# Optimization experiments

Hardware: AMD Instinct MI355X
Metric: run time of the kernel (lower is better)

The kernel has to match this reference:

```python
import jax, jax.numpy as jnp
import numpy as np

CHUNK = 128


def setup_inputs() -> dict:
    key = jax.random.key(0)
    ks = jax.random.split(key, 10)
    B, L, d, n = 4, 2048, 192, 64
    sd = 1.0 / np.sqrt(d)
    return {
        "x": jax.random.normal(ks[0], (B, L, d), dtype=jnp.float32),
        "A_log": -jnp.log(2.0) + 0.1 * jax.random.normal(ks[1], (d,), dtype=jnp.float32),
        "W_B": sd * jax.random.normal(ks[2], (n, d), dtype=jnp.float32),
        "W_C": sd * jax.random.normal(ks[3], (n, d), dtype=jnp.float32),
        "W_dt": sd * jax.random.normal(ks[4], (d, d), dtype=jnp.float32),
        "b_dt": 0.1 * jax.random.normal(ks[5], (d,), dtype=jnp.float32),
        "W_xp": sd * jax.random.normal(ks[6], (2 * d, d), dtype=jnp.float32),
        "b_xp": 0.1 * jax.random.normal(ks[7], (2 * d,), dtype=jnp.float32),
        "W_out": sd * jax.random.normal(ks[8], (d, d), dtype=jnp.float32),
        "b_out": 0.1 * jax.random.normal(ks[9], (d,), dtype=jnp.float32),
    }


def reference(x, A_log, W_B, W_C, W_dt, b_dt, W_xp, b_xp, W_out, b_out):
    p = CHUNK
    b, l, d = x.shape
    n = W_B.shape[0]
    pad = (-l) % p
    xp = jnp.pad(x, ((0, 0), (0, pad), (0, 0))) if pad > 0 else x
    c = xp.shape[1] // p

    A = -jnp.exp(A_log)                                   # (d,)
    proj = xp @ W_xp.T + b_xp                             # (b, Lp, 2d)
    x_bar, z = jnp.split(proj, 2, axis=-1)
    Bm = x_bar @ W_B.T                                    # (b, Lp, n)
    Cm = x_bar @ W_C.T                                    # (b, Lp, n)
    dt = jax.nn.softplus(x_bar @ W_dt.T + b_dt)           # (b, Lp, d)
    A_bar = jnp.exp(dt * A)                               # (b, Lp, d)

    resh = lambda t: t.reshape(b, c, p, t.shape[-1])
    xc, Bc, Cc, Ac = resh(x_bar), resh(Bm), resh(Cm), resh(A_bar)

    # intra-chunk: masked decay matrix M[b,c,i,j,d]
    log_A = jnp.log(jnp.abs(Ac) + 1e-8)
    la_cum = jnp.cumsum(log_A, axis=2)                    # (b,c,p,d)
    log_M = la_cum[:, :, :, None, :] - la_cum[:, :, None, :, :]
    causal = jnp.tril(jnp.ones((p, p), dtype=x.dtype))
    M = jnp.exp(log_M) * causal[None, None, :, :, None]   # (b,c,p,p,d)
    G = jnp.einsum('bcin,bcjn->bcij', Cc, Bc)             # C_i . B_j
    # same math as einsum('bcpn,bcpnd->bcpd', C, einsum('bcijd,bcjnd->bcind', M, B x))
    y_intra = jnp.einsum('bcij,bcijd,bcjd->bcid', G, M, xc)

    # inter-chunk recurrence over chunk states
    chunk_A = jnp.prod(Ac, axis=2)                        # (b,c,d)
    chunk_states = jnp.einsum('bcpn,bcpd->bcnd', Bc, xc * Ac)

    def step(state, inp):
        ca, cs = inp                                       # (b,d), (b,n,d)
        return state * ca[:, None, :] + cs, state          # emit state BEFORE update

    _, prev = jax.lax.scan(
        step,
        jnp.zeros((b, n, d), dtype=x.dtype),
        (jnp.moveaxis(chunk_A, 1, 0), jnp.moveaxis(chunk_states, 1, 0)),
    )
    prev = jnp.moveaxis(prev, 0, 1)                       # (b,c,n,d)
    y_inter = jnp.einsum('bcpn,bcnd->bcpd', Cc, prev)

    y = (y_intra + y_inter).reshape(b, c * p, d)[:, :l]
    y = y * jax.nn.silu(z[:, :l])
    return y @ W_out.T + b_out
```

## Files before the change

kernel.cpp:

```cpp
#include <hip/hip_runtime.h>
#include <math.h>

#define TOK      8192
#define DIM      192
#define NST      64
#define PCHUNK   128
#define NCHUNKS  64
#define CPB      16
#define BATCH    4
#define SUB      32
#define NSUB     4
#define NG2      2
#define NPG2     32

typedef __attribute__((ext_vector_type(8))) short  bf16x8;
typedef __attribute__((ext_vector_type(4))) float  f32x4;

__device__ __forceinline__ unsigned short f2bf(float f) {
    unsigned int u = __float_as_uint(f);
    u += 0x7fff + ((u >> 16) & 1);
    return (unsigned short)(u >> 16);
}

__global__ __launch_bounds__(256)
void cast_kernel(const float* __restrict__ x,   const float* __restrict__ Wxp,
                 const float* __restrict__ WB,  const float* __restrict__ WC,
                 const float* __restrict__ Wdt, const float* __restrict__ Wout,
                 unsigned short* __restrict__ xb,     unsigned short* __restrict__ wxpb,
                 unsigned short* __restrict__ wbcdtb, unsigned short* __restrict__ woutb)
{
    int u = blockIdx.x * 256 + threadIdx.x;
    const float* src; unsigned short* dst; int idx;
    if      (u < 393216) { src = x;    dst = xb;             idx = u; }
    else if (u < 411648) { src = Wxp;  dst = wxpb;           idx = u - 393216; }
    else if (u < 414720) { src = WB;   dst = wbcdtb;         idx = u - 411648; }
    else if (u < 417792) { src = WC;   dst = wbcdtb + 12288; idx = u - 414720; }
    else if (u < 427008) { src = Wdt;  dst = wbcdtb + 24576; idx = u - 417792; }
    else if (u < 436224) { src = Wout; dst = woutb;          idx = u - 427008; }
    else return;
    float4 v = *(const float4*)(src + (size_t)idx * 4);
    ushort4 r; r.x = f2bf(v.x); r.y = f2bf(v.y); r.z = f2bf(v.z); r.w = f2bf(v.w);
    *(ushort4*)(dst + (size_t)idx * 4) = r;
}

__device__ __forceinline__
void mfma_64x64(const unsigned short* __restrict__ X, int ldx,
                const unsigned short* __restrict__ W, int K,
                int m_wave, int n0, int lr, int kg, f32x4 acc[4][4])
{
    for (int k0 = 0; k0 < K; k0 += 32) {
        bf16x8 af[4], bfr[4];
        #pragma unroll
        for (int mi = 0; mi < 4; ++mi)
            af[mi] = *(const bf16x8*)(X + (size_t)(m_wave + mi*16 + lr) * ldx + k0 + kg*8);
        #pragma unroll
        for (int ni = 0; ni < 4; ++ni)
            bfr[ni] = *(const bf16x8*)(W + (size_t)(n0 + ni*16 + lr) * K + k0 + kg*8);
        #pragma unroll
        for (int mi = 0; mi < 4; ++mi)
            #pragma unroll
            for (int ni = 0; ni < 4; ++ni)
                acc[mi][ni] = __builtin_amdgcn_mfma_f32_16x16x32_bf16(
                                  af[mi], bfr[ni], acc[mi][ni], 0, 0, 0);
    }
}

__global__ __launch_bounds__(256)
void proj_gemm(const unsigned short* __restrict__ xb,
               const unsigned short* __restrict__ wxpb,
               const float* __restrict__ b_xp,
               float* __restrict__ proj, unsigned short* __restrict__ projb)
{
    const int lane = threadIdx.x & 63, wave = threadIdx.x >> 6;
    const int m_wave = blockIdx.x * 256 + wave * 64;
    const int n0 = blockIdx.y * 64;
    const int lr = lane & 15, kg = lane >> 4;
    f32x4 acc[4][4] = {};
    mfma_64x64(xb, DIM, wxpb, DIM, m_wave, n0, lr, kg, acc);
    #pragma unroll
    for (int ni = 0; ni < 4; ++ni) {
        int col = n0 + ni*16 + lr;
        float bias = b_xp[col];
        #pragma unroll
        for (int mi = 0; mi < 4; ++mi)
            #pragma unroll
            for (int r = 0; r < 4; ++r) {
                int row = m_wave + mi*16 + kg*4 + r;
                float v = acc[mi][ni][r] + bias;
                proj [(size_t)row * 384 + col] = v;
                projb[(size_t)row * 384 + col] = f2bf(v);
            }
    }
}

__global__ __launch_bounds__(256)
void bcdt_gemm(const unsigned short* __restrict__ projb,
               const unsigned short* __restrict__ wbcdtb,
               const float* __restrict__ b_dt, const float* __restrict__ A_log,
               float* __restrict__ BC, float* __restrict__ Abar)
{
    const int lane = threadIdx.x & 63, wave = threadIdx.x >> 6;
    const int m_wave = blockIdx.x * 256 + wave * 64;
    const int n0 = blockIdx.y * 64;
    const int lr = lane & 15, kg = lane >> 4;
    f32x4 acc[4][4] = {};
    mfma_64x64(projb, 384, wbcdtb, DIM, m_wave, n0, lr, kg, acc);
    if (n0 < 128) {
        #pragma unroll
        for (int ni = 0; ni < 4; ++ni) {
            int col = n0 + ni*16 + lr;
            #pragma unroll
            for (int mi = 0; mi < 4; ++mi)
                #pragma unroll
                for (int r = 0; r < 4; ++r) {
                    int row = m_wave + mi*16 + kg*4 + r;
                    BC[(size_t)row * 128 + col] = acc[mi][ni][r];
                }
        }
    } else {
        #pragma unroll
        for (int ni = 0; ni < 4; ++ni) {
            int c2 = n0 - 128 + ni*16 + lr;
            float bias = b_dt[c2];
            float Av = -expf(A_log[c2]);
            #pragma unroll
            for (int mi = 0; mi < 4; ++mi)
                #pragma unroll
                for (int r = 0; r < 4; ++r) {
                    int row = m_wave + mi*16 + kg*4 + r;
                    float v = acc[mi][ni][r] + bias;
                    float sp = (v > 20.f) ? v : log1pf(expf(v));
                    Abar[(size_t)row * DIM + c2] = expf(sp * Av);
                }
        }
    }
}

__global__ __launch_bounds__(256)
void out_gemm(const unsigned short* __restrict__ ygb,
              const unsigned short* __restrict__ woutb,
              const float* __restrict__ b_out, float* __restrict__ out)
{
    const int lane = threadIdx.x & 63, wave = threadIdx.x >> 6;
    const int m_wave = blockIdx.x * 256 + wave * 64;
    const int n0 = blockIdx.y * 64;
    const int lr = lane & 15, kg = lane >> 4;
    f32x4 acc[4][4] = {};
    mfma_64x64(ygb, DIM, woutb, DIM, m_wave, n0, lr, kg, acc);
    #pragma unroll
    for (int ni = 0; ni < 4; ++ni) {
        int col = n0 + ni*16 + lr;
        float bias = b_out[col];
        #pragma unroll
        for (int mi = 0; mi < 4; ++mi)
            #pragma unroll
            for (int r = 0; r < 4; ++r) {
                int row = m_wave + mi*16 + kg*4 + r;
                out[(size_t)row * DIM + col] = acc[mi][ni][r] + bias;
            }
    }
}

__global__ __launch_bounds__(192)
void state_kernel(const float* __restrict__ proj,
                  const float* __restrict__ Abar,
                  const float* __restrict__ Bm,
                  float* __restrict__ S,
                  float* __restrict__ R,
                  float* __restrict__ dprod)
{
    int bc = blockIdx.x, s = blockIdx.y, g = blockIdx.z;
    int dd = threadIdx.x;
    int t0 = bc * PCHUNK + s * SUB;
    __shared__ float Bs[SUB][NPG2];
    for (int idx = threadIdx.x; idx < SUB * NPG2; idx += 192) {
        int i = idx >> 5, j = idx & 31;
        Bs[i][j] = Bm[(size_t)(t0 + i) * 128 + g * NPG2 + j];
    }
    __syncthreads();
    float H[NPG2] = {}, Rr[NPG2] = {};
    float cp = 1.f;
    float a_cur = fabsf(Abar[(size_t)t0 * DIM + dd]) + 1e-8f;
    float x_cur = proj[(size_t)t0 * 384 + dd];
    for (int i = 0; i < SUB; ++i) {
        float a_nxt = 0.f, x_nxt = 0.f;
        if (i + 1 < SUB) {
            a_nxt = fabsf(Abar[(size_t)(t0 + i + 1) * DIM + dd]) + 1e-8f;
            x_nxt = proj[(size_t)(t0 + i + 1) * 384 + dd];
        }
        cp *= a_cur;
        #pragma unroll
        for (int j = 0; j < NPG2; ++j) {
            float u = Bs[i][j] * x_cur;
            H[j]  = fmaf(a_cur, H[j], u);
            Rr[j] = fmaf(u, a_cur, Rr[j]);
        }
        a_cur = a_nxt; x_cur = x_nxt;
    }
    size_t base = (((size_t)(bc * NSUB + s)) * NST + g * NPG2) * DIM + dd;
    #pragma unroll
    for (int j = 0; j < NPG2; ++j) {
        S[base + (size_t)j * DIM] = H[j];
        R[base + (size_t)j * DIM] = Rr[j];
    }
    if (g == 0) dprod[(size_t)(bc * NSUB + s) * DIM + dd] = cp;
}

__global__ __launch_bounds__(256)
void scan_kernel(const float* __restrict__ dprod,
                 const float* __restrict__ R,
                 float* __restrict__ prev)
{
    int v = blockIdx.x * 256 + threadIdx.x;
    if (v >= BATCH * NST * 48) return;
    int dd = (v % 48) * 4;
    int nn = (v / 48) % NST;
    int b  = v / (48 * NST);
    const size_t Q2 = (size_t)NST * DIM;
    float4 st = {0.f, 0.f, 0.f, 0.f};
    for (int c = 0; c < CPB; ++c) {
        int bc = b * CPB + c;
        size_t so = ((size_t)(bc * NSUB) * NST + nn) * DIM + dd;
        float4 Rs = {0.f, 0.f, 0.f, 0.f};
        float4 cA = {1.f, 1.f, 1.f, 1.f};
        #pragma unroll
        for (int s = 0; s < NSUB; ++s) {
            float4 dp = *(const float4*)(dprod + (size_t)(bc * NSUB + s) * DIM + dd);
            float4 Rv = *(const float4*)(R + so + (size_t)s * Q2);
            cA.x *= dp.x; cA.y *= dp.y; cA.z *= dp.z; cA.w *= dp.w;
            Rs.x += Rv.x; Rs.y += Rv.y; Rs.z += Rv.z; Rs.w += Rv.w;
        }
        size_t po = ((size_t)bc * NST + nn) * DIM + dd;
        *(float4*)(prev + po) = st;
        st.x = fmaf(st.x, cA.x, Rs.x);
        st.y = fmaf(st.y, cA.y, Rs.y);
        st.z = fmaf(st.z, cA.z, Rs.z);
        st.w = fmaf(st.w, cA.w, Rs.w);
    }
}

__global__ __launch_bounds__(192)
void intra_kernel(const float* __restrict__ proj,
                  const float* __restrict__ Abar,
                  const float* __restrict__ Bm,
                  const float* __restrict__ Cm,
                  const float* __restrict__ prev,
                  const float* __restrict__ S,
                  const float* __restrict__ dprod,
                  float* __restrict__ p_y)
{
    int bc = blockIdx.x, s = blockIdx.y, g = blockIdx.z;
    int dd = threadIdx.x;
    int t0 = bc * PCHUNK + s * SUB;
    __shared__ float Bs[SUB][NPG2];
    __shared__ float Cs[SUB][NPG2];
    for (int idx = threadIdx.x; idx < SUB * NPG2; idx += 192) {
        int i = idx >> 5, j = idx & 31;
        Bs[i][j] = Bm[(size_t)(t0 + i) * 128 + g * NPG2 + j];
        Cs[i][j] = Cm[(size_t)(t0 + i) * 128 + g * NPG2 + j];
    }
    float H[NPG2] = {}, P[NPG2];
    for (int k = 0; k < s; ++k) {
        float dpk = dprod[(size_t)(bc * NSUB + k) * DIM + dd];
        size_t sb = (((size_t)(bc * NSUB + k)) * NST + g * NPG2) * DIM + dd;
        #pragma unroll
        for (int j = 0; j < NPG2; ++j)
            H[j] = fmaf(H[j], dpk, S[sb + (size_t)j * DIM]);
    }
    #pragma unroll
    for (int j = 0; j < NPG2; ++j)
        P[j] = prev[((size_t)bc * NST + g * NPG2 + j) * DIM + dd];
    __syncthreads();

    float a_cur = fabsf(Abar[(size_t)t0 * DIM + dd]) + 1e-8f;
    float x_cur = proj[(size_t)t0 * 384 + dd];
    for (int i = 0; i < SUB; ++i) {
        int t = t0 + i;
        float a_nxt = 0.f, x_nxt = 0.f;
        if (i + 1 < SUB) {
            a_nxt = fabsf(Abar[(size_t)(t + 1) * DIM + dd]) + 1e-8f;
            x_nxt = proj[(size_t)(t + 1) * 384 + dd];
        }
        float ya[4] = {0.f, 0.f, 0.f, 0.f};
        #pragma unroll
        for (int j = 0; j < NPG2; ++j) {
            float u = Bs[i][j] * x_cur;
            H[j] = fmaf(a_cur, H[j], u);
            ya[j & 3] = fmaf(Cs[i][j], H[j] + P[j], ya[j & 3]);
        }
        p_y[((size_t)g * TOK + t) * DIM + dd] = (ya[0] + ya[1]) + (ya[2] + ya[3]);
        a_cur = a_nxt; x_cur = x_nxt;
    }
}

__global__ __launch_bounds__(256)
void gate_kernel(const float* __restrict__ p_y,
                 const float* __restrict__ proj,
                 unsigned short* __restrict__ ygb)
{
    int v = blockIdx.x * 256 + threadIdx.x;
    if (v >= TOK * 48) return;
    int t = v / 48;
    int dd = (v % 48) * 4;
    const size_t Q = (size_t)TOK * DIM;
    size_t off = (size_t)t * DIM + dd;
    float4 y0 = *(const float4*)(p_y + off);
    float4 y1 = *(const float4*)(p_y + off + Q);
    float4 z  = *(const float4*)(proj + (size_t)t * 384 + DIM + dd);
    ushort4 r;
    r.x = f2bf((y0.x+y1.x) * (z.x / (1.f + expf(-z.x))));
    r.y = f2bf((y0.y+y1.y) * (z.y / (1.f + expf(-z.y))));
    r.z = f2bf((y0.z+y1.z) * (z.z / (1.f + expf(-z.z))));
    r.w = f2bf((y0.w+y1.w) * (z.w / (1.f + expf(-z.w))));
    *(ushort4*)(ygb + off) = r;
}

extern "C" void kernel_launch(void* const* d_in, const int* in_sizes, int n_in,
                              void* d_out, int out_size, void* d_ws, size_t ws_size,
                              hipStream_t stream)
{
    (void)in_sizes; (void)n_in; (void)out_size; (void)ws_size;
    const float* x     = (const float*)d_in[0];
    const float* A_log = (const float*)d_in[1];
    const float* W_B   = (const float*)d_in[2];
    const float* W_C   = (const float*)d_in[3];
    const float* W_dt  = (const float*)d_in[4];
    const float* b_dt  = (const float*)d_in[5];
    const float* W_xp  = (const float*)d_in[6];
    const float* b_xp  = (const float*)d_in[7];
    const float* W_out = (const float*)d_in[8];
    const float* b_out = (const float*)d_in[9];
    float* out = (float*)d_out;

    char* w = (char*)d_ws;
    auto take = [&](size_t bytes) { char* p = w; w += (bytes + 255) & ~(size_t)255; return p; };
    float*          proj   = (float*)         take((size_t)TOK*384*4);
    unsigned short* projb  = (unsigned short*)take((size_t)TOK*384*2);
    unsigned short* xb     = (unsigned short*)take((size_t)TOK*DIM*2);
    unsigned short* wxpb   = (unsigned short*)take((size_t)384*DIM*2);
    unsigned short* wbcdtb = (unsigned short*)take((size_t)320*DIM*2);
    unsigned short* woutb  = (unsigned short*)take((size_t)DIM*DIM*2);
    float*          BC     = (float*)         take((size_t)TOK*128*4);
    float*          Abar   = (float*)         take((size_t)TOK*DIM*4);
    float*          dprod  = (float*)         take((size_t)NCHUNKS*NSUB*DIM*4);
    float*          prev   = (float*)         take((size_t)NCHUNKS*NST*DIM*4);
    float*          Sarr   = (float*)         take((size_t)NCHUNKS*NSUB*NST*DIM*4);
    float*          Rarr   = (float*)         take((size_t)NCHUNKS*NSUB*NST*DIM*4);
    float*          p_y    = (float*)         take((size_t)NG2*TOK*DIM*4);
    unsigned short* ygb    = (unsigned short*)take((size_t)TOK*DIM*2);
    const float* Bm = BC;
    const float* Cm = BC + 64;

    dim3 blk(256);

    cast_kernel<<<dim3((436224 + 255)/256), blk, 0, stream>>>(
        x, W_xp, W_B, W_C, W_dt, W_out, xb, wxpb, wbcdtb, woutb);
    proj_gemm<<<dim3(TOK/256, 384/64), blk, 0, stream>>>(xb, wxpb, b_xp, proj, projb);
    bcdt_gemm<<<dim3(TOK/256, 320/64), blk, 0, stream>>>(projb, wbcdtb, b_dt, A_log, BC, Abar);
    state_kernel<<<dim3(NCHUNKS, NSUB, NG2), dim3(192), 0, stream>>>(
        proj, Abar, Bm, Sarr, Rarr, dprod);
    scan_kernel<<<dim3((BATCH*NST*48 + 255)/256), blk, 0, stream>>>(dprod, Rarr, prev);
    intra_kernel<<<dim3(NCHUNKS, NSUB, NG2), dim3(192), 0, stream>>>(
        proj, Abar, Bm, Cm, prev, Sarr, dprod, p_y);
    gate_kernel<<<dim3((TOK*48 + 255)/256), blk, 0, stream>>>(p_y, proj, ygb);
    out_gemm<<<dim3(TOK/256, DIM/64), blk, 0, stream>>>(ygb, woutb, b_out, out);
}
```

Baseline: 188.3 us.

## Split SSM state groups four ways, parallelize chunk reductions, store partials in bf16

Doubles the number of state-dimension groups in the state and intra kernels (16 states per block instead of 32), which doubles the grid and reduces per-thread register pressure. The per-chunk sum of sub-chunk contributions is moved out of the serial scan into a separate fully parallel reduce kernel. Shared-memory staging now uses float4 loads. Intra-chunk partial outputs are written as bf16 and summed over four groups in the gate kernel. This adds another launch and lowers the precision of the partial sums.

```diff
diff --git a/kernel.cpp b/kernel.cpp
--- a/kernel.cpp
+++ b/kernel.cpp
@@ -10,8 +10,8 @@
 #define BATCH    4
 #define SUB      32
 #define NSUB     4
-#define NG2      2
-#define NPG2     32
+#define NG       4
+#define NPG      16
 
 typedef __attribute__((ext_vector_type(8))) short  bf16x8;
 typedef __attribute__((ext_vector_type(4))) float  f32x4;
@@ -20,6 +20,9 @@
     unsigned int u = __float_as_uint(f);
     u += 0x7fff + ((u >> 16) & 1);
     return (unsigned short)(u >> 16);
+}
+__device__ __forceinline__ float bf2f(unsigned short h) {
+    return __uint_as_float(((unsigned int)h) << 16);
 }
 
 __global__ __launch_bounds__(256)
@@ -172,13 +175,14 @@
     int bc = blockIdx.x, s = blockIdx.y, g = blockIdx.z;
     int dd = threadIdx.x;
     int t0 = bc * PCHUNK + s * SUB;
-    __shared__ float Bs[SUB][NPG2];
-    for (int idx = threadIdx.x; idx < SUB * NPG2; idx += 192) {
-        int i = idx >> 5, j = idx & 31;
-        Bs[i][j] = Bm[(size_t)(t0 + i) * 128 + g * NPG2 + j];
+    __shared__ float Bs[SUB][NPG];
+    if (threadIdx.x < SUB * NPG / 4) {
+        int row = threadIdx.x >> 2, c4 = threadIdx.x & 3;
+        *(float4*)&Bs[row][c4 * 4] =
+            *(const float4*)(Bm + (size_t)(t0 + row) * 128 + g * NPG + c4 * 4);
     }
     __syncthreads();
-    float H[NPG2] = {}, Rr[NPG2] = {};
+    float H[NPG] = {}, Rr[NPG] = {};
     float cp = 1.f;
     float a_cur = fabsf(Abar[(size_t)t0 * DIM + dd]) + 1e-8f;
     float x_cur = proj[(size_t)t0 * 384 + dd];
@@ -189,17 +193,23 @@
             x_nxt = proj[(size_t)(t0 + i + 1) * 384 + dd];
         }
         cp *= a_cur;
-        #pragma unroll
-        for (int j = 0; j < NPG2; ++j) {
-            float u = Bs[i][j] * x_cur;
+        float4 b0 = *(const float4*)&Bs[i][0];
+        float4 b1 = *(const float4*)&Bs[i][4];
+        float4 b2 = *(const float4*)&Bs[i][8];
+        float4 b3 = *(const float4*)&Bs[i][12];
+        float bb[NPG] = {b0.x,b0.y,b0.z,b0.w, b1.x,b1.y,b1.z,b1.w,
+                         b2.x,b2.y,b2.z,b2.w, b3.x,b3.y,b3.z,b3.w};
+        #pragma unroll
+        for (int j = 0; j < NPG; ++j) {
+            float u = bb[j] * x_cur;
             H[j]  = fmaf(a_cur, H[j], u);
             Rr[j] = fmaf(u, a_cur, Rr[j]);
         }
         a_cur = a_nxt; x_cur = x_nxt;
     }
-    size_t base = (((size_t)(bc * NSUB + s)) * NST + g * NPG2) * DIM + dd;
+    size_t base = (((size_t)(bc * NSUB + s)) * NST + g * NPG) * DIM + dd;
     #pragma unroll
-    for (int j = 0; j < NPG2; ++j) {
+    for (int j = 0; j < NPG; ++j) {
         S[base + (size_t)j * DIM] = H[j];
         R[base + (size_t)j * DIM] = Rr[j];
     }
@@ -207,8 +217,43 @@
 }
 
 __global__ __launch_bounds__(256)
-void scan_kernel(const float* __restrict__ dprod,
-                 const float* __restrict__ R,
+void reduce_kernel(const float* __restrict__ dprod,
+                   const float* __restrict__ R,
+                   float* __restrict__ cA,
+                   float* __restrict__ Rsum)
+{
+    int u = blockIdx.x * 256 + threadIdx.x;
+    const int NR = NCHUNKS * NST * 48;
+    if (u < NR) {
+        int dd = (u % 48) * 4;
+        int nn = (u / 48) % NST;
+        int bc = u / (48 * NST);
+        const size_t Q2 = (size_t)NST * DIM;
+        size_t so = ((size_t)(bc * NSUB) * NST + nn) * DIM + dd;
+        float4 acc = {0.f, 0.f, 0.f, 0.f};
+        #pragma unroll
+        for (int s = 0; s < NSUB; ++s) {
+            float4 v = *(const float4*)(R + so + (size_t)s * Q2);
+            acc.x += v.x; acc.y += v.y; acc.z += v.z; acc.w += v.w;
+        }
+        *(float4*)(Rsum + ((size_t)bc * NST + nn) * DIM + dd) = acc;
+    } else if (u < NR + NCHUNKS * 48) {
+        int v = u - NR;
+        int dd = (v % 48) * 4;
+        int bc = v / 48;
+        float4 acc = {1.f, 1.f, 1.f, 1.f};
+        #pragma unroll
+        for (int s = 0; s < NSUB; ++s) {
+            float4 dp = *(const float4*)(dprod + (size_t)(bc * NSUB + s) * DIM + dd);
+            acc.x *= dp.x; acc.y *= dp.y; acc.z *= dp.z; acc.w *= dp.w;
+        }
+        *(float4*)(cA + (size_t)bc * DIM + dd) = acc;
+    }
+}
+
+__global__ __launch_bounds__(256)
+void scan_kernel(const float* __restrict__ cA,
+                 const float* __restrict__ Rsum,
                  float* __restrict__ prev)
 {
     int v = blockIdx.x * 256 + threadIdx.x;
@@ -216,26 +261,23 @@
     int dd = (v % 48) * 4;
     int nn = (v / 48) % NST;
     int b  = v / (48 * NST);
-    const size_t Q2 = (size_t)NST * DIM;
+    int bc0 = b * CPB;
     float4 st = {0.f, 0.f, 0.f, 0.f};
+    float4 a_cur = *(const float4*)(cA + (size_t)bc0 * DIM + dd);
+    float4 r_cur = *(const float4*)(Rsum + ((size_t)bc0 * NST + nn) * DIM + dd);
     for (int c = 0; c < CPB; ++c) {
-        int bc = b * CPB + c;
-        size_t so = ((size_t)(bc * NSUB) * NST + nn) * DIM + dd;
-        float4 Rs = {0.f, 0.f, 0.f, 0.f};
-        float4 cA = {1.f, 1.f, 1.f, 1.f};
-        #pragma unroll
-        for (int s = 0; s < NSUB; ++s) {
-            float4 dp = *(const float4*)(dprod + (size_t)(bc * NSUB + s) * DIM + dd);
-            float4 Rv = *(const float4*)(R + so + (size_t)s * Q2);
-            cA.x *= dp.x; cA.y *= dp.y; cA.z *= dp.z; cA.w *= dp.w;
-            Rs.x += Rv.x; Rs.y += Rv.y; Rs.z += Rv.z; Rs.w += Rv.w;
-        }
-        size_t po = ((size_t)bc * NST + nn) * DIM + dd;
-        *(float4*)(prev + po) = st;
-        st.x = fmaf(st.x, cA.x, Rs.x);
-        st.y = fmaf(st.y, cA.y, Rs.y);
-        st.z = fmaf(st.z, cA.z, Rs.z);
-        st.w = fmaf(st.w, cA.w, Rs.w);
+        int bc = bc0 + c;
+        float4 a_nxt = {0,0,0,0}, r_nxt = {0,0,0,0};
+        if (c + 1 < CPB) {
+            a_nxt = *(const float4*)(cA + (size_t)(bc + 1) * DIM + dd);
+            r_nxt = *(const float4*)(Rsum + ((size_t)(bc + 1) * NST + nn) * DIM + dd);
+        }
+        *(float4*)(prev + ((size_t)bc * NST + nn) * DIM + dd) = st;
+        st.x = fmaf(st.x, a_cur.x, r_cur.x);
+        st.y = fmaf(st.y, a_cur.y, r_cur.y);
+        st.z = fmaf(st.z, a_cur.z, r_cur.z);
+        st.w = fmaf(st.w, a_cur.w, r_cur.w);
+        a_cur = a_nxt; r_cur = r_nxt;
     }
 }
 
@@ -247,29 +289,39 @@
                   const float* __restrict__ prev,
                   const float* __restrict__ S,
                   const float* __restrict__ dprod,
-                  float* __restrict__ p_y)
+                  unsigned short* __restrict__ p_y)
 {
     int bc = blockIdx.x, s = blockIdx.y, g = blockIdx.z;
     int dd = threadIdx.x;
     int t0 = bc * PCHUNK + s * SUB;
-    __shared__ float Bs[SUB][NPG2];
-    __shared__ float Cs[SUB][NPG2];
-    for (int idx = threadIdx.x; idx < SUB * NPG2; idx += 192) {
-        int i = idx >> 5, j = idx & 31;
-        Bs[i][j] = Bm[(size_t)(t0 + i) * 128 + g * NPG2 + j];
-        Cs[i][j] = Cm[(size_t)(t0 + i) * 128 + g * NPG2 + j];
-    }
-    float H[NPG2] = {}, P[NPG2];
+    __shared__ float Bs[SUB][NPG];
+    __shared__ float Cs[SUB][NPG];
+    if (threadIdx.x < SUB * NPG / 2) {
+    }
+    {
+        int nunits = SUB * NPG / 4;
+        for (int idx = threadIdx.x; idx < 2 * nunits; idx += 192) {
+            int m = idx >= nunits;
+            int q = idx - m * nunits;
+            int row = q >> 2, c4 = q & 3;
+            const float* src = (m ? Cm : Bm) + (size_t)(t0 + row) * 128
+                             + (m ? 64 : 0) + g * NPG + c4 * 4;
+            float4 v = *(const float4*)src;
+            if (m) *(float4*)&Cs[row][c4 * 4] = v;
+            else   *(float4*)&Bs[row][c4 * 4] = v;
+        }
+    }
+    float H[NPG] = {}, P[NPG];
     for (int k = 0; k < s; ++k) {
         float dpk = dprod[(size_t)(bc * NSUB + k) * DIM + dd];
-        size_t sb = (((size_t)(bc * NSUB + k)) * NST + g * NPG2) * DIM + dd;
-        #pragma unroll
-        for (int j = 0; j < NPG2; ++j)
+        size_t sb = (((size_t)(bc * NSUB + k)) * NST + g * NPG) * DIM + dd;
+        #pragma unroll
+        for (int j = 0; j < NPG; ++j)
             H[j] = fmaf(H[j], dpk, S[sb + (size_t)j * DIM]);
     }
     #pragma unroll
-    for (int j = 0; j < NPG2; ++j)
-        P[j] = prev[((size_t)bc * NST + g * NPG2 + j) * DIM + dd];
+    for (int j = 0; j < NPG; ++j)
+        P[j] = prev[((size_t)bc * NST + g * NPG + j) * DIM + dd];
     __syncthreads();
 
     float a_cur = fabsf(Abar[(size_t)t0 * DIM + dd]) + 1e-8f;
@@ -281,20 +333,31 @@
             a_nxt = fabsf(Abar[(size_t)(t + 1) * DIM + dd]) + 1e-8f;
             x_nxt = proj[(size_t)(t + 1) * 384 + dd];
         }
+        float4 b0 = *(const float4*)&Bs[i][0];
+        float4 b1 = *(const float4*)&Bs[i][4];
+        float4 b2 = *(const float4*)&Bs[i][8];
+        float4 b3 = *(const float4*)&Bs[i][12];
+        float4 c0 = *(const float4*)&Cs[i][0];
+        float4 c1 = *(const float4*)&Cs[i][4];
+        float4 c2 = *(const float4*)&Cs[i][8];
+        float4 c3 = *(const float4*)&Cs[i][12];
+        float bb[NPG] = {b0.x,b0.y,b0.z,b0.w, b1.x,b1.y,b1.z,b1.w,
+                         b2.x,b2.y,b2.z,b2.w, b3.x,b3.y,b3.z,b3.w};
+        float cc[NPG] = {c0.x,c0.y,c0.z,c0.w, c1.x,c1.y,c1.z,c1.w,
+                         c2.x,c2.y,c2.z,c2.w, c3.x,c3.y,c3.z,c3.w};
         float ya[4] = {0.f, 0.f, 0.f, 0.f};
         #pragma unroll
-        for (int j = 0; j < NPG2; ++j) {
-            float u = Bs[i][j] * x_cur;
-            H[j] = fmaf(a_cur, H[j], u);
-            ya[j & 3] = fmaf(Cs[i][j], H[j] + P[j], ya[j & 3]);
-        }
-        p_y[((size_t)g * TOK + t) * DIM + dd] = (ya[0] + ya[1]) + (ya[2] + ya[3]);
+        for (int j = 0; j < NPG; ++j) {
+            H[j] = fmaf(a_cur, H[j], bb[j] * x_cur);
+            ya[j & 3] = fmaf(cc[j], H[j] + P[j], ya[j & 3]);
+        }
+        p_y[((size_t)g * TOK + t) * DIM + dd] = f2bf((ya[0] + ya[1]) + (ya[2] + ya[3]));
         a_cur = a_nxt; x_cur = x_nxt;
     }
 }
 
 __global__ __launch_bounds__(256)
-void gate_kernel(const float* __restrict__ p_y,
+void gate_kernel(const unsigned short* __restrict__ p_y,
                  const float* __restrict__ proj,
                  unsigned short* __restrict__ ygb)
 {
@@ -304,14 +367,19 @@
     int dd = (v % 48) * 4;
     const size_t Q = (size_t)TOK * DIM;
     size_t off = (size_t)t * DIM + dd;
-    float4 y0 = *(const float4*)(p_y + off);
-    float4 y1 = *(const float4*)(p_y + off + Q);
-    float4 z  = *(const float4*)(proj + (size_t)t * 384 + DIM + dd);
+    float acc[4] = {0.f, 0.f, 0.f, 0.f};
+    #pragma unroll
+    for (int gidx = 0; gidx < NG; ++gidx) {
+        ushort4 y = *(const ushort4*)(p_y + off + (size_t)gidx * Q);
+        acc[0] += bf2f(y.x); acc[1] += bf2f(y.y);
+        acc[2] += bf2f(y.z); acc[3] += bf2f(y.w);
+    }
+    float4 z = *(const float4*)(proj + (size_t)t * 384 + DIM + dd);
     ushort4 r;
-    r.x = f2bf((y0.x+y1.x) * (z.x / (1.f + expf(-z.x))));
-    r.y = f2bf((y0.y+y1.y) * (z.y / (1.f + expf(-z.y))));
-    r.z = f2bf((y0.z+y1.z) * (z.z / (1.f + expf(-z.z))));
-    r.w = f2bf((y0.w+y1.w) * (z.w / (1.f + expf(-z.w))));
+    r.x = f2bf(acc[0] * (z.x / (1.f + expf(-z.x))));
+    r.y = f2bf(acc[1] * (z.y / (1.f + expf(-z.y))));
+    r.z = f2bf(acc[2] * (z.z / (1.f + expf(-z.z))));
+    r.w = f2bf(acc[3] * (z.w / (1.f + expf(-z.w))));
     *(ushort4*)(ygb + off) = r;
 }
 
@@ -343,24 +411,27 @@
     float*          BC     = (float*)         take((size_t)TOK*128*4);
     float*          Abar   = (float*)         take((size_t)TOK*DIM*4);
     float*          dprod  = (float*)         take((size_t)NCHUNKS*NSUB*DIM*4);
+    float*          cAc    = (float*)         take((size_t)NCHUNKS*DIM*4);
     float*          prev   = (float*)         take((size_t)NCHUNKS*NST*DIM*4);
+    float*          Rsum   = (float*)         take((size_t)NCHUNKS*NST*DIM*4);
     float*          Sarr   = (float*)         take((size_t)NCHUNKS*NSUB*NST*DIM*4);
     float*          Rarr   = (float*)         take((size_t)NCHUNKS*NSUB*NST*DIM*4);
-    float*          p_y    = (float*)         take((size_t)NG2*TOK*DIM*4);
+    unsigned short* p_y    = (unsigned short*)take((size_t)NG*TOK*DIM*2);
     unsigned short* ygb    = (unsigned short*)take((size_t)TOK*DIM*2);
     const float* Bm = BC;
-    const float* Cm = BC + 64;
-
+    const float* Cm = BC;
     dim3 blk(256);
 
     cast_kernel<<<dim3((436224 + 255)/256), blk, 0, stream>>>(
         x, W_xp, W_B, W_C, W_dt, W_out, xb, wxpb, wbcdtb, woutb);
     proj_gemm<<<dim3(TOK/256, 384/64), blk, 0, stream>>>(xb, wxpb, b_xp, proj, projb);
     bcdt_gemm<<<dim3(TOK/256, 320/64), blk, 0, stream>>>(projb, wbcdtb, b_dt, A_log, BC, Abar);
-    state_kernel<<<dim3(NCHUNKS, NSUB, NG2), dim3(192), 0, stream>>>(
+    state_kernel<<<dim3(NCHUNKS, NSUB, NG), dim3(192), 0, stream>>>(
         proj, Abar, Bm, Sarr, Rarr, dprod);
-    scan_kernel<<<dim3((BATCH*NST*48 + 255)/256), blk, 0, stream>>>(dprod, Rarr, prev);
-    intra_kernel<<<dim3(NCHUNKS, NSUB, NG2), dim3(192), 0, stream>>>(
+    reduce_kernel<<<dim3((NCHUNKS*NST*48 + NCHUNKS*48 + 255)/256), blk, 0, stream>>>(
+        dprod, Rarr, cAc, Rsum);
+    scan_kernel<<<dim3((BATCH*NST*48 + 255)/256), blk, 0, stream>>>(cAc, Rsum, prev);
+    intra_kernel<<<dim3(NCHUNKS, NSUB, NG), dim3(192), 0, stream>>>(
         proj, Abar, Bm, Cm, prev, Sarr, dprod, p_y);
     gate_kernel<<<dim3((TOK*48 + 255)/256), blk, 0, stream>>>(p_y, proj, ygb);
     out_gemm<<<dim3(TOK/256, DIM/64), blk, 0, stream>>>(ygb, woutb, b_out, out);
```

Measured after the change: 179.2 us. 1.05x faster.
